# Optimization experiments

Measured on AMD Instinct MI355X. Metric: run time of the kernel, lower is better.

## Reference

```python
import jax, jax.numpy as jnp
import numpy as np

B, T, D_MODEL = 2, 2048, 2048
N, H, R = 1024, 16, 512
DH = 128          # mem_head_dim (even, fully rotated: rope_dim == DH)
MLAT = 128        # mem_latent_dim
TOPK = 64
EPS = 1e-6
ROPE_BASE = 10000.0


def _rms_norm(x, w):
    var = jnp.mean(jnp.square(x), axis=-1, keepdims=True)
    return x * jax.lax.rsqrt(var + EPS) * w


def _rotate_half(x):
    x1, x2 = jnp.split(x, 2, axis=-1)
    return jnp.concatenate([-x2, x1], axis=-1)


def _apply_rope(x, positions):
    # x: [B, H, L, DH], positions: [L] -> cos/sin [1, 1, L, DH]
    inv_freq = 1.0 / (ROPE_BASE ** (jnp.arange(0, DH, 2, dtype=jnp.float32) / DH))
    freqs = positions.astype(jnp.float32)[:, None] * inv_freq  # [L, DH/2]
    emb = jnp.concatenate([freqs, freqs], axis=-1)             # [L, DH]
    cos = jnp.cos(emb)[None, None].astype(x.dtype)
    sin = jnp.sin(emb)[None, None].astype(x.dtype)
    return x * cos + _rotate_half(x) * sin


def setup_inputs() -> dict:
    key = jax.random.key(0)
    ks = jax.random.split(key, 16)
    s = 0.02
    return {
        "x": jax.random.normal(ks[0], (B, T, D_MODEL), jnp.float32),
        "snapshots": jax.random.normal(ks[1], (B, N, H, R), jnp.float32),
        "snap_positions": jnp.sort(jax.random.randint(ks[2], (N,), 0, T)),
        "token_offset": 0,
        "Wq_down": jax.random.normal(ks[3], (D_MODEL, MLAT), jnp.float32) * s,
        "Wq_up": jax.random.normal(ks[4], (MLAT, H * DH), jnp.float32) * s,
        "Wg_down": jax.random.normal(ks[5], (D_MODEL, MLAT), jnp.float32) * s,
        "Wg_up": jax.random.normal(ks[6], (MLAT, H * DH), jnp.float32) * s,
        "Wo_down": jax.random.normal(ks[7], (H * DH, MLAT), jnp.float32) * s,
        "Wo_up": jax.random.normal(ks[8], (MLAT, D_MODEL), jnp.float32) * s,
        "Wk_up": jax.random.normal(ks[9], (R, DH), jnp.float32) * s,
        "Wv_up": jax.random.normal(ks[10], (R, DH), jnp.float32) * s,
        "q_norm_w": jnp.ones((DH,), jnp.float32),
        "k_norm_w": jnp.ones((DH,), jnp.float32),
        "sink_logit": jnp.zeros((H,), jnp.float32),
    }


def reference(x, snapshots, snap_positions, token_offset,
              Wq_down, Wq_up, Wg_down, Wg_up, Wo_down, Wo_up,
              Wk_up, Wv_up, q_norm_w, k_norm_w, sink_logit):
    b, t, d = x.shape
    _, n, h, r = snapshots.shape
    dh = DH

    # Q path: down/up projection, per-head RMSNorm -> [B, H, T, DH]
    q = ((x @ Wq_down) @ Wq_up).reshape(b, t, h, dh)
    q = _rms_norm(q, q_norm_w).transpose(0, 2, 1, 3)

    # K/V from snapshot latents: [B, N, H, DH] -> [B, H, N, DH]
    k = _rms_norm(snapshots @ Wk_up, k_norm_w).transpose(0, 2, 1, 3)
    v = (snapshots @ Wv_up).transpose(0, 2, 1, 3)

    # dual RoPE: Q by absolute token position, K by snapshot end position
    t_abs = token_offset + jnp.arange(t)
    q = _apply_rope(q, t_abs)
    k = _apply_rope(k, snap_positions)

    scores = jnp.einsum('bhtd,bhnd->bhtn', q, k) / jnp.sqrt(jnp.asarray(dh, q.dtype))

    # causal mask: snapshot strictly before token
    valid = (snap_positions[None, :] < t_abs[:, None])[None, None]  # [1,1,T,N]
    neg_inf = jnp.asarray(-jnp.inf, scores.dtype)
    scores = jnp.where(valid, scores, neg_inf)

    # causal top-k: keep entries >= k-th largest per (b,h,t)
    k_sel = min(TOPK, n)
    if k_sel < n:
        top_vals, _ = jax.lax.top_k(scores, k_sel)
        kth = top_vals[..., -1:]
        scores = jnp.where(scores >= kth, scores, neg_inf)

    # attention sink: extra learned logit per head
    sink = jnp.broadcast_to(sink_logit.astype(jnp.float32)[None, :, None, None], (b, h, t, 1))
    aug = jnp.concatenate([scores.astype(jnp.float32), sink], axis=-1)
    weights = jax.nn.softmax(aug, axis=-1)[..., :n].astype(v.dtype)

    out = jnp.einsum('bhtn,bhnd->bhtd', weights, v)
    out = out.transpose(0, 2, 1, 3).reshape(b, t, h * dh)

    gate = jax.nn.sigmoid((x @ Wg_down) @ Wg_up)
    out = out * gate
    out = (out @ Wo_down) @ Wo_up
    return out
```

## Files before the change

kernel.cpp:

```cpp
#include <hip/hip_runtime.h>

typedef unsigned short u16;
typedef unsigned int u32;
typedef __attribute__((ext_vector_type(8))) short bf16x8;
typedef __attribute__((ext_vector_type(8))) _Float16 f16x8;
typedef __attribute__((ext_vector_type(4))) float f32x4;

__device__ __forceinline__ float b2f(u16 u) {
  union { u32 i; float f; } v; v.i = ((u32)u) << 16; return v.f;
}
__device__ __forceinline__ u16 f2b(float f) {
  u32 u = __builtin_bit_cast(u32, f);
  u32 r = u + 0x7FFFu + ((u >> 16) & 1u);
  return (u16)(r >> 16);
}
__device__ __forceinline__ u16 f2h(float f) {
  return __builtin_bit_cast(u16, (_Float16)f);
}
__device__ __forceinline__ float h2f(u16 u) {
  return (float)__builtin_bit_cast(_Float16, u);
}
__device__ __forceinline__ float wsum(float v) {
  #pragma unroll
  for (int o = 32; o; o >>= 1) v += __shfl_xor(v, o);
  return v;
}

__global__ void k_detect(const u32* x, int* flag) {
  int lane = threadIdx.x;
  u32 w = x[lane * 131 + 7];
  float v = b2f((u16)(w & 0xFFFF));
  float a = fabsf(v);
  bool sane = (a > 1e-3f) && (a < 100.0f);
  unsigned long long m = __ballot(sane);
  if (lane == 0) flag[0] = (__popcll(m) >= 32) ? 0 : 1;
}

__global__ __launch_bounds__(256)
void k_tab(const int* spos, const int* tok, float2* qtab, float2* ktab, int* nmaxg) {
  if (blockIdx.x == 768) {
    int t = threadIdx.x;
    if (t < 128) {
      int lim = tok[0] + t * 16 + 15;
      int lo = 0, hi = 1024;
      #pragma unroll 1
      while (lo < hi) { int mid = (lo + hi) >> 1; if (spos[mid] < lim) lo = mid + 1; else hi = mid; }
      nmaxg[t] = lo;
    }
    return;
  }
  int id = blockIdx.x * 4 + (threadIdx.x >> 6);
  int lane = threadIdx.x & 63;
  float invf = __expf(-(float)lane * (9.210340371976184f / 64.0f));
  if (id < 2048) {
    float pos = (float)(tok[0] + id);
    float sn, cs; sincosf(pos * invf, &sn, &cs);
    qtab[id * 64 + lane] = make_float2(cs, sn);
  } else {
    int n = id - 2048;
    float pos = (float)spos[n];
    float sn, cs; sincosf(pos * invf, &sn, &cs);
    ktab[n * 64 + lane] = make_float2(cs, sn);
  }
}

struct WtArgs {
  const void* s[8];
  const void* vq; const void* vk; const void* vs;
};
__global__ __launch_bounds__(256)
void k_wtrans_all(WtArgs a, u16* wb, const int* flag) {
  __shared__ u16 Ts[64][66];
  int id = blockIdx.x, t = threadIdx.x, dt = flag[0];
  if (id == 416) {
    u16* dq = wb + 1703936; u16* dk = wb + 1704064; u16* ds = wb + 1704192;
    if (t < 128) dq[t] = dt ? f2b(((const float*)a.vq)[t]) : ((const u16*)a.vq)[t];
    else if (t < 256) dk[t-128] = dt ? f2b(((const float*)a.vk)[t-128]) : ((const u16*)a.vk)[t-128];
    if (t < 16) ds[t] = dt ? f2b(((const float*)a.vs)[t]) : ((const u16*)a.vs)[t];
    return;
  }
  const int cum[9] = {0,64,128,144,160,224,288,352,416};
  const int gsh[8] = {1,1,1,1,5,5,1,5};
  const int Ks[8]  = {2048,2048,512,512,128,128,2048,128};
  const int Ns[8]  = {128,128,128,128,2048,2048,128,2048};
  const unsigned dsts[8] = {0,262144,524288,589824,655360,917504,1179648,1441792};
  int seg = 0;
  #pragma unroll
  for (int i = 0; i < 7; ++i) seg += (id >= cum[i+1]);
  int rel = id - cum[seg];
  int bx = rel & ((1 << gsh[seg]) - 1), by = rel >> gsh[seg];
  int K = Ks[seg], N = Ns[seg];
  const void* src = a.s[seg];
  u16* dst = wb + dsts[seg];
  int col0 = bx * 64, k0 = by * 64;
  int lr = t >> 4, lc = (t & 15) * 4;
  if (dt) {
    #pragma unroll
    for (int p = 0; p < 4; ++p) {
      int kr = lr + p * 16;
      float4 v = *(const float4*)((const float*)src + (size_t)(k0 + kr) * N + col0 + lc);
      Ts[kr][lc+0] = f2b(v.x); Ts[kr][lc+1] = f2b(v.y);
      Ts[kr][lc+2] = f2b(v.z); Ts[kr][lc+3] = f2b(v.w);
    }
  } else {
    #pragma unroll
    for (int p = 0; p < 4; ++p) {
      int kr = lr + p * 16;
      uint2 v = *(const uint2*)((const u16*)src + (size_t)(k0 + kr) * N + col0 + lc);
      *(uint2*)&Ts[kr][lc] = v;
    }
  }
  __syncthreads();
  int col = t >> 2, ks = (t & 3) * 16;
  u16 tmp[16];
  #pragma unroll
  for (int i = 0; i < 16; ++i) tmp[i] = Ts[ks + i][col];
  u16* dp = dst + (size_t)(col0 + col) * K + k0 + ks;
  *(uint4*)dp = *(uint4*)&tmp[0];
  *(uint4*)(dp + 8) = *(uint4*)&tmp[8];
}

template<int JW>
__device__ __forceinline__ void skinny_body(const void* A, const u16* BT, u16* C0, u16* C1,
    int K, bool a32, int m0, int tid, u16 (*As)[40]) {
  int wave = tid >> 6, lane = tid & 63, quad = lane >> 4, l16 = lane & 15;
  f32x4 acc[JW];
  #pragma unroll
  for (int j = 0; j < JW; ++j) acc[j] = (f32x4){0.f,0.f,0.f,0.f};
  int row32 = tid >> 4, kp32 = (tid & 15) * 2;
  int row16 = tid >> 2, kp16 = (tid & 3) * 8;
  float2 pf32 = {};
  uint4 pf16 = {};
  if (a32) pf32 = *(const float2*)((const float*)A + (size_t)(m0+row32)*K + kp32);
  else if (tid < 64) pf16 = *(const uint4*)((const u16*)A + (size_t)(m0+row16)*K + kp16);
  uint4 bf[JW];
  #pragma unroll
  for (int j = 0; j < JW; ++j) {
    int col = wave*(JW*16) + j*16 + l16;
    bf[j] = *(const uint4*)(BT + (size_t)col*K + quad*8);
  }
  for (int k0 = 0; k0 < K; k0 += 32) {
    if (a32) { As[row32][kp32] = f2b(pf32.x); As[row32][kp32+1] = f2b(pf32.y); }
    else if (tid < 64) *(uint4*)&As[row16][kp16] = pf16;
    __syncthreads();
    int k1 = k0 + 32;
    uint4 bn[JW];
    if (k1 < K) {
      if (a32) pf32 = *(const float2*)((const float*)A + (size_t)(m0+row32)*K + k1 + kp32);
      else if (tid < 64) pf16 = *(const uint4*)((const u16*)A + (size_t)(m0+row16)*K + k1 + kp16);
      #pragma unroll
      for (int j = 0; j < JW; ++j) {
        int col = wave*(JW*16) + j*16 + l16;
        bn[j] = *(const uint4*)(BT + (size_t)col*K + k1 + quad*8);
      }
    }
    bf16x8 af = *(const bf16x8*)&As[l16][quad*8];
    #pragma unroll
    for (int j = 0; j < JW; ++j)
      acc[j] = __builtin_amdgcn_mfma_f32_16x16x32_bf16(af, __builtin_bit_cast(bf16x8, bf[j]), acc[j], 0, 0, 0);
    __syncthreads();
    #pragma unroll
    for (int j = 0; j < JW; ++j) bf[j] = bn[j];
  }
  #pragma unroll
  for (int j = 0; j < JW; ++j) {
    int col = wave*(JW*16) + j*16 + l16;
    u16* Cp = (col < 128) ? C0 : C1;
    int cc = col & 127;
    #pragma unroll
    for (int r = 0; r < 4; ++r)
      Cp[(size_t)(m0 + quad*4 + r)*128 + cc] = f2b(acc[j][r]);
  }
}

__device__ __forceinline__ void gemm_up_body(const u16* A, const u16* BT, void* C, int ldc,
    bool o32, int m0, int n0, int tid, u16 (*As)[40]) {
  int wave = tid >> 6, lane = tid & 63, quad = lane >> 4, l16 = lane & 15;
  f32x4 acc[4] = {};
  int row = tid >> 2, kp = (tid & 3) * 8;
  uint4 pa = *(const uint4*)(A + (size_t)(m0+row)*128 + kp);
  uint4 bf[4];
  #pragma unroll
  for (int j = 0; j < 4; ++j)
    bf[j] = *(const uint4*)(BT + (size_t)(n0 + j*16 + l16)*128 + quad*8);
  #pragma unroll
  for (int k0 = 0; k0 < 128; k0 += 32) {
    *(uint4*)&As[row][kp] = pa;
    __syncthreads();
    uint4 bn[4];
    if (k0 < 96) {
      pa = *(const uint4*)(A + (size_t)(m0+row)*128 + k0 + 32 + kp);
      #pragma unroll
      for (int j = 0; j < 4; ++j)
        bn[j] = *(const uint4*)(BT + (size_t)(n0 + j*16 + l16)*128 + k0 + 32 + quad*8);
    }
    bf16x8 af = *(const bf16x8*)&As[wave*16 + l16][quad*8];
    #pragma unroll
    for (int j = 0; j < 4; ++j)
      acc[j] = __builtin_amdgcn_mfma_f32_16x16x32_bf16(af, __builtin_bit_cast(bf16x8, bf[j]), acc[j], 0, 0, 0);
    __syncthreads();
    #pragma unroll
    for (int j = 0; j < 4; ++j) bf[j] = bn[j];
  }
  #pragma unroll
  for (int j = 0; j < 4; ++j) {
    #pragma unroll
    for (int r = 0; r < 4; ++r) {
      size_t ci = (size_t)(m0 + wave*16 + quad*4 + r)*ldc + n0 + j*16 + l16;
      float v = acc[j][r];
      if (o32) ((float*)C)[ci] = v; else ((u16*)C)[ci] = f2b(v);
    }
  }
}

__device__ __forceinline__ void kpost_body(const u16* kraw, u16* kT, const u16* kw,
                                           const float2* ktab, int rel, int tid) {
  int wave = tid >> 6, lane = tid & 63;
  int rr = rel * 4 + wave;
  int n = (rr >> 4) & 1023, b = rr >> 14, h = rr & 15;
  size_t base = (size_t)rr * 128;
  float x0 = b2f(kraw[base + lane]);
  float x1 = b2f(kraw[base + lane + 64]);
  float ss = wsum(x0*x0 + x1*x1);
  float inv = rsqrtf(ss * (1.0f/128.0f) + 1e-6f);
  float y0 = x0 * inv * b2f(kw[lane]);
  float y1 = x1 * inv * b2f(kw[lane + 64]);
  float2 cs2 = ktab[n * 64 + lane];
  size_t ob = ((size_t)(b*16 + h) * 1024 + n) * 128;
  kT[ob + lane]      = f2b(y0*cs2.x - y1*cs2.y);
  kT[ob + lane + 64] = f2b(y1*cs2.x + y0*cs2.y);
}

__device__ __forceinline__ void vtrans_body(const u16* vraw, u16* vtt, int bid, int t,
                                            u16 (*Vs)[136]) {
  int ng = bid & 15, bh = bid >> 4;
  int b = bh >> 4, h = bh & 15;
  int n0 = ng * 64;
  int li = t >> 4, seg = (t & 15) * 8;
  #pragma unroll
  for (int p = 0; p < 4; ++p) {
    int i = li + p * 16;
    size_t row = (size_t)(b*1024 + n0 + i) * 16 + h;
    *(uint4*)&Vs[i][seg] = *(const uint4*)(vraw + row*128 + seg);
  }
  __syncthreads();
  int dh = t >> 1, nh = (t & 1) * 32;
  u16 outv[32];
  #pragma unroll
  for (int i = 0; i < 32; ++i) outv[i] = f2h(b2f(Vs[nh + i][dh]));
  u16* dst = vtt + ((size_t)bh * 128 + dh) * 1024 + n0 + nh;
  *(uint4*)(dst)      = *(uint4*)&outv[0];
  *(uint4*)(dst + 8)  = *(uint4*)&outv[8];
  *(uint4*)(dst + 16) = *(uint4*)&outv[16];
  *(uint4*)(dst + 24) = *(uint4*)&outv[24];
}

__global__ __launch_bounds__(256)
void k_down_all(const void* x, const void* snap, const u16* BdT, const u16* BkvT,
                u16* qlat, u16* glat, u16* kraw, u16* vraw, const int* flag) {
  __shared__ u16 As[16][40];
  int id = blockIdx.x;
  bool a32 = flag[0] != 0;
  if (id < 256) skinny_body<4>(x, BdT, qlat, glat, 2048, a32, id*16, threadIdx.x, As);
  else          skinny_body<4>(snap, BkvT, kraw, vraw, 512, a32, (id-256)*16, threadIdx.x, As);
}

__global__ __launch_bounds__(256)
void k_mid_all(const u16* qlat, const u16* glat, const u16* WquT, const u16* WguT,
               u16* qraw, u16* graw, const u16* kraw, u16* kT, const u16* vraw, u16* vtt,
               const u16* ckw, const float2* ktab, const int* flag) {
  __shared__ u16 smem[64*136];
  int id = blockIdx.x, tid = threadIdx.x;
  if (id < 4096) {
    u16 (*As)[40] = (u16 (*)[40])smem;
    int rel = id & 2047;
    const u16* A  = (id < 2048) ? qlat : glat;
    const u16* BT = (id < 2048) ? WquT : WguT;
    u16* C        = (id < 2048) ? qraw : graw;
    gemm_up_body(A, BT, C, 2048, false, (rel >> 5) * 64, (rel & 31) * 64, tid, As);
  } else if (id < 12288) {
    kpost_body(kraw, kT, ckw, ktab, id - 4096, tid);
  } else {
    vtrans_body(vraw, vtt, id - 12288, tid, (u16 (*)[136])smem);
  }
}

__global__ __launch_bounds__(256)
void k_olat(const u16* Ao, const u16* WodT, u16* olat, const int* flag) {
  __shared__ u16 As[16][40];
  skinny_body<2>(Ao, WodT, olat, olat, 2048, false, blockIdx.x*16, threadIdx.x, As);
}

__global__ __launch_bounds__(256)
void k_gemm_up(const u16* A, const u16* BT, void* C, int ldc, const int* flag, int out_dyn) {
  __shared__ u16 As[64][40];
  gemm_up_body(A, BT, C, ldc, out_dyn && flag[0], blockIdx.y*64, blockIdx.x*64, threadIdx.x, As);
}

template<int NJ>
__device__ __forceinline__ void attn_phase2(char* scB, float* rzb, int tl0, int lane,
                                            int nmax, float sinkv, bool do_search) {
  int c0 = lane * 8;
  #pragma unroll 1
  for (int half = 0; half < 2; ++half) {
    float sv[2][NJ]; int key[2][NJ];
    #pragma unroll
    for (int s2 = 0; s2 < 2; ++s2) {
      int tl = tl0 + half*2 + s2;
      int sxor = (tl & 7) << 4;
      const char* rowp = scB + tl*2048;
      uint4 r0 = *(const uint4*)(rowp + ((lane*16) ^ sxor));
      #pragma unroll
      for (int j = 0; j < 8; ++j)
        sv[s2][j] = (c0 + j < nmax) ? h2f(((const u16*)&r0)[j]) : -INFINITY;
      if constexpr (NJ == 16) {
        uint4 r1 = *(const uint4*)(rowp + (1024 + ((lane*16) ^ sxor)));
        #pragma unroll
        for (int j = 0; j < 8; ++j)
          sv[s2][j+8] = (c0 + j + 512 < nmax) ? h2f(((const u16*)&r1)[j]) : -INFINITY;
      }
    }
    float mx[2];
    #pragma unroll
    for (int s2 = 0; s2 < 2; ++s2) {
      float m = -INFINITY;
      #pragma unroll
      for (int j = 0; j < NJ; ++j) {
        float f = sv[s2][j];
        m = fmaxf(m, f);
        float fs = fminf(fmaxf(f * 256.0f + 2048.0f, 0.0f), 4095.0f);
        key[s2][j] = (int)fs;
      }
      mx[s2] = m;
    }
    #pragma unroll
    for (int os = 32; os; os >>= 1) {
      mx[0] = fmaxf(mx[0], __shfl_xor(mx[0], os));
      mx[1] = fmaxf(mx[1], __shfl_xor(mx[1], os));
    }
    int lo2[2] = {0, 0};
    if (do_search) {
      int hi2[2] = {4096, 4096};
      #pragma unroll 1
      for (int it = 0; it < 12; ++it) {
        #pragma unroll
        for (int s2 = 0; s2 < 2; ++s2) {
          int mid = (lo2[s2] + hi2[s2]) >> 1;
          int c = 0;
          #pragma unroll
          for (int j = 0; j < NJ; ++j) c += (int)__popcll(__ballot(key[s2][j] >= mid));
          if (c >= 64) lo2[s2] = mid; else hi2[s2] = mid;
        }
      }
    }
    float m2[2], zp[2];
    u16 wq[2][16];
    #pragma unroll
    for (int s2 = 0; s2 < 2; ++s2) {
      m2[s2] = fmaxf(mx[s2], sinkv);
      float z = 0.f;
      #pragma unroll
      for (int j = 0; j < NJ; ++j) {
        float e = (key[s2][j] >= lo2[s2] && sv[s2][j] > -1e37f) ? __expf(sv[s2][j] - m2[s2]) : 0.f;
        z += e;
        wq[s2][j] = f2h(e);
      }
      zp[s2] = z;
    }
    #pragma unroll
    for (int os = 32; os; os >>= 1) {
      zp[0] += __shfl_xor(zp[0], os);
      zp[1] += __shfl_xor(zp[1], os);
    }
    #pragma unroll
    for (int s2 = 0; s2 < 2; ++s2) {
      int tl = tl0 + half*2 + s2;
      float Z = zp[s2] + __expf(sinkv - m2[s2]);
      if (lane == 0) rzb[tl] = 1.0f / Z;
      int sxor = (tl & 7) << 4;
      char* rowp = scB + tl*2048;
      *(uint4*)(rowp + ((lane*16) ^ sxor)) = *(uint4*)&wq[s2][0];
      if constexpr (NJ == 16)
        *(uint4*)(rowp + (1024 + ((lane*16) ^ sxor))) = *(uint4*)&wq[s2][8];
    }
  }
}

__global__ __launch_bounds__(256, 5)
void k_attn(const u16* qraw, const u16* kT, const u16* vtt, const u16* graw,
            const int* spos, const int* tok, const u16* sink, const u16* qw,
            const float2* qtab, const int* nmaxg, float* rzg, u16* o) {
  __shared__ u16 sc[16*1024];
  char* scB = (char*)sc;
  u16 (*Qs)[136] = (u16 (*)[136])sc;

  int tid = threadIdx.x;
  int wave = tid >> 6, lane = tid & 63, quad = lane >> 4, l16 = lane & 15;
  int bid0 = blockIdx.x;
  int bid = (bid0 & 7) * 512 + (bid0 >> 3);
  int tile = bid & 127, bh = bid >> 7;
  int h = bh & 15, b = bh >> 4;
  int t0 = tile * 16;
  int tok0 = tok[0];
  float* rzb = rzg + bid * 16;

  {
    float qw0 = b2f(qw[lane]), qw1 = b2f(qw[lane + 64]);
    #pragma unroll 1
    for (int s = 0; s < 4; ++s) {
      int i = wave*4 + s;
      size_t base = ((size_t)(b*2048 + t0 + i))*2048 + h*128;
      float x0 = b2f(qraw[base + lane]);
      float x1 = b2f(qraw[base + lane + 64]);
      float ss = wsum(x0*x0 + x1*x1);
      float inv = rsqrtf(ss * (1.0f/128.0f) + 1e-6f);
      float y0 = x0 * inv * qw0;
      float y1 = x1 * inv * qw1;
      float2 cs2 = qtab[(size_t)(t0 + i)*64 + lane];
      Qs[i][lane]      = f2b(y0*cs2.x - y1*cs2.y);
      Qs[i][lane + 64] = f2b(y1*cs2.x + y0*cs2.y);
    }
  }
  __syncthreads();

  int nmax = nmaxg[tile];
  int pmax = (nmax + 63) >> 6;
  int kkmax = (nmax + 31) >> 5;

  bf16x8 af[4];
  #pragma unroll
  for (int ks = 0; ks < 4; ++ks) af[ks] = *(const bf16x8*)&Qs[l16][ks*32 + quad*8];
  __syncthreads();

  const u16* kTb = kT + (size_t)bh * 131072;
  int nrow = wave*16 + l16;
  uint4 kf[4];
  int pn = 0;
  if (pmax > 0) {
    const u16* kr = kTb + (size_t)nrow * 128 + quad*8;
    #pragma unroll
    for (int ks = 0; ks < 4; ++ks) kf[ks] = *(const uint4*)(kr + ks*32);
    pn = spos[nrow];
  }
  int lim0 = tok0 + t0;
  #pragma unroll 1
  for (int p = 0; p < pmax; ++p) {
    uint4 kn[4];
    int pn_next = 0;
    if (p + 1 < pmax) {
      const u16* kr = kTb + (size_t)((p+1)*64 + nrow) * 128 + quad*8;
      #pragma unroll
      for (int ks = 0; ks < 4; ++ks) kn[ks] = *(const uint4*)(kr + ks*32);
      pn_next = spos[(p+1)*64 + nrow];
    }
    f32x4 c = {};
    __builtin_amdgcn_s_setprio(1);
    #pragma unroll
    for (int ks = 0; ks < 4; ++ks)
      c = __builtin_amdgcn_mfma_f32_16x16x32_bf16(af[ks], __builtin_bit_cast(bf16x8, kf[ks]), c, 0, 0, 0);
    __builtin_amdgcn_s_setprio(0);
    int n = p*64 + nrow;
    #pragma unroll
    for (int r = 0; r < 4; ++r) {
      int t = quad*4 + r;
      float s = c[r] * 0.08838834764831845f;
      if (pn >= lim0 + t) s = -INFINITY;
      *(u16*)(scB + ((t*2048 + n*2) ^ ((t&7)<<4))) = f2h(s);
    }
    #pragma unroll
    for (int ks = 0; ks < 4; ++ks) kf[ks] = kn[ks];
    pn = pn_next;
  }
  __syncthreads();

  float sinkv = b2f(sink[h]);

  int tl0 = wave*4;
  bool do_search = (nmax > 64);
  if (nmax > 512) attn_phase2<16>(scB, rzb, tl0, lane, nmax, sinkv, do_search);
  else            attn_phase2<8> (scB, rzb, tl0, lane, nmax, sinkv, do_search);
  __syncthreads();

  int dh0 = wave * 32;
  float rz4[4];
  u16 g0r[4], g1r[4];
  #pragma unroll
  for (int r = 0; r < 4; ++r) {
    int t = quad*4 + r;
    rz4[r] = rzb[t];
    size_t oi = ((size_t)(b*2048 + t0 + t))*2048 + h*128 + dh0 + l16;
    g0r[r] = graw[oi];
    g1r[r] = graw[oi + 16];
  }

  const u16* vbase = vtt + (size_t)bh * 131072;
  const u16* vr0 = vbase + (size_t)(dh0 + l16)*1024 + quad*8;
  const u16* vr1 = vbase + (size_t)(dh0 + 16 + l16)*1024 + quad*8;
  f32x4 acc0 = {}, acc1 = {};
  uint4 vf0 = *(const uint4*)vr0;
  uint4 vf1 = *(const uint4*)vr1;
  int axor = (l16&7) << 4;
  const char* arow = scB + l16*2048;
  #pragma unroll 1
  for (int kk = 0; kk < kkmax; ++kk) {
    uint4 vn0, vn1;
    if (kk + 1 < kkmax) {
      vn0 = *(const uint4*)(vr0 + (kk+1)*32);
      vn1 = *(const uint4*)(vr1 + (kk+1)*32);
    }
    f16x8 a = *(const f16x8*)(arow + ((kk*64 + quad*16) ^ axor));
    __builtin_amdgcn_s_setprio(1);
    acc0 = __builtin_amdgcn_mfma_f32_16x16x32_f16(a, __builtin_bit_cast(f16x8, vf0), acc0, 0, 0, 0);
    acc1 = __builtin_amdgcn_mfma_f32_16x16x32_f16(a, __builtin_bit_cast(f16x8, vf1), acc1, 0, 0, 0);
    __builtin_amdgcn_s_setprio(0);
    vf0 = vn0; vf1 = vn1;
  }

  #pragma unroll
  for (int r = 0; r < 4; ++r) {
    int t = quad*4 + r;
    size_t oi = ((size_t)(b*2048 + t0 + t))*2048 + h*128 + dh0 + l16;
    float g0 = 1.0f / (1.0f + __expf(-b2f(g0r[r])));
    float g1 = 1.0f / (1.0f + __expf(-b2f(g1r[r])));
    o[oi] = f2b(acc0[r] * rz4[r] * g0);
    o[oi + 16] = f2b(acc1[r] * rz4[r] * g1);
  }
}

extern "C" void kernel_launch(void* const* d_in, const int* in_sizes, int n_in,
                              void* d_out, int out_size, void* d_ws, size_t ws_size,
                              hipStream_t stream) {
  char* ws = (char*)d_ws;
  int* flag = (int*)(ws + 0);
  u16* wb = (u16*)(ws + 4096);

  u16* BdT  = wb + 0;
  u16* BkvT = wb + 524288;
  u16* WquT = wb + 655360;
  u16* WguT = wb + 917504;
  u16* WodT = wb + 1179648;
  u16* WouT = wb + 1441792;
  u16* cqw  = wb + 1703936;
  u16* ckw  = wb + 1704064;
  u16* csink= wb + 1704192;

  const size_t O_QLAT = 4198400;
  const size_t O_GLAT = 5246976;
  const size_t O_QRAW = 6295552;
  const size_t O_GRAW = 23072768;
  const size_t O_KRAW = 39849984;
  const size_t O_VRAW = 48238592;
  const size_t O_KT   = 56627200;
  const size_t O_VTT  = 65015808;
  const size_t O_QTAB = 73404416;
  const size_t O_KTAB = 74452992;
  const size_t O_NMAX = 74977280;

  const int* spos = (const int*)d_in[2];
  const int* tok  = (const int*)d_in[3];

  k_detect<<<1, 64, 0, stream>>>((const u32*)d_in[0], flag);

  k_tab<<<769, 256, 0, stream>>>(spos, tok, (float2*)(ws + O_QTAB), (float2*)(ws + O_KTAB),
      (int*)(ws + O_NMAX));

  WtArgs wa;
  wa.s[0] = d_in[4];  wa.s[1] = d_in[6];  wa.s[2] = d_in[10]; wa.s[3] = d_in[11];
  wa.s[4] = d_in[5];  wa.s[5] = d_in[7];  wa.s[6] = d_in[8];  wa.s[7] = d_in[9];
  wa.vq = d_in[12]; wa.vk = d_in[13]; wa.vs = d_in[14];
  k_wtrans_all<<<417, 256, 0, stream>>>(wa, wb, flag);

  k_down_all<<<2304, 256, 0, stream>>>(d_in[0], d_in[1], BdT, BkvT,
      (u16*)(ws + O_QLAT), (u16*)(ws + O_GLAT), (u16*)(ws + O_KRAW), (u16*)(ws + O_VRAW), flag);

  k_mid_all<<<12800, 256, 0, stream>>>((const u16*)(ws + O_QLAT), (const u16*)(ws + O_GLAT),
      WquT, WguT, (u16*)(ws + O_QRAW), (u16*)(ws + O_GRAW),
      (const u16*)(ws + O_KRAW), (u16*)(ws + O_KT), (const u16*)(ws + O_VRAW), (u16*)(ws + O_VTT),
      ckw, (const float2*)(ws + O_KTAB), flag);

  k_attn<<<4096, 256, 0, stream>>>((const u16*)(ws + O_QRAW), (const u16*)(ws + O_KT),
      (const u16*)(ws + O_VTT), (const u16*)(ws + O_GRAW), spos, tok, csink, cqw,
      (const float2*)(ws + O_QTAB), (const int*)(ws + O_NMAX),
      (float*)(ws + O_GLAT), (u16*)(ws + O_GRAW));

  k_olat<<<256, 256, 0, stream>>>((const u16*)(ws + O_GRAW), WodT, (u16*)(ws + O_QLAT), flag);
  k_gemm_up<<<dim3(32,64), 256, 0, stream>>>((const u16*)(ws + O_QLAT), WouT, d_out, 2048, flag, 1);
}
```

Before: 507.1 us.

## Halve attention tile to 8 tokens, split-K olat GEMM, fuse table kernel

The attention kernel now handles 8 query tokens per block instead of 16. It uses half the shared memory, launches twice as many blocks and raises the occupancy hint from 5 to 8. Its MFMA tiles are still 16 wide, so half the rows are duplicates and wasted. The skinny o-latent GEMM is split four ways along K into fp32 partials, followed by a small reduction kernel, to get more parallelism. The rope/nmax table kernel is merged into the weight-transpose launch to save one launch. The nmax granularity changes to 8 tokens to match the new tile size.

```diff
diff --git a/kernel.cpp b/kernel.cpp
--- a/kernel.cpp
+++ b/kernel.cpp
@@ -36,42 +36,40 @@
   if (lane == 0) flag[0] = (__popcll(m) >= 32) ? 0 : 1;
 }
 
-__global__ __launch_bounds__(256)
-void k_tab(const int* spos, const int* tok, float2* qtab, float2* ktab, int* nmaxg) {
-  if (blockIdx.x == 768) {
-    int t = threadIdx.x;
-    if (t < 128) {
-      int lim = tok[0] + t * 16 + 15;
-      int lo = 0, hi = 1024;
-      #pragma unroll 1
-      while (lo < hi) { int mid = (lo + hi) >> 1; if (spos[mid] < lim) lo = mid + 1; else hi = mid; }
-      nmaxg[t] = lo;
-    }
-    return;
-  }
-  int id = blockIdx.x * 4 + (threadIdx.x >> 6);
-  int lane = threadIdx.x & 63;
-  float invf = __expf(-(float)lane * (9.210340371976184f / 64.0f));
-  if (id < 2048) {
-    float pos = (float)(tok[0] + id);
-    float sn, cs; sincosf(pos * invf, &sn, &cs);
-    qtab[id * 64 + lane] = make_float2(cs, sn);
-  } else {
-    int n = id - 2048;
-    float pos = (float)spos[n];
-    float sn, cs; sincosf(pos * invf, &sn, &cs);
-    ktab[n * 64 + lane] = make_float2(cs, sn);
-  }
-}
-
 struct WtArgs {
   const void* s[8];
   const void* vq; const void* vk; const void* vs;
 };
 __global__ __launch_bounds__(256)
-void k_wtrans_all(WtArgs a, u16* wb, const int* flag) {
+void k_wtab(WtArgs a, u16* wb, const int* flag, const int* spos, const int* tok,
+            float2* qtab, float2* ktab, int* nmaxg) {
   __shared__ u16 Ts[64][66];
-  int id = blockIdx.x, t = threadIdx.x, dt = flag[0];
+  int id = blockIdx.x, t = threadIdx.x;
+  if (id >= 417) {
+    if (id == 1185) {
+      int lim = tok[0] + t * 8 + 7;
+      int lo = 0, hi = 1024;
+      #pragma unroll 1
+      while (lo < hi) { int mid = (lo + hi) >> 1; if (spos[mid] < lim) lo = mid + 1; else hi = mid; }
+      nmaxg[t] = lo;
+      return;
+    }
+    int rid = (id - 417) * 4 + (t >> 6);
+    int lane = t & 63;
+    float invf = __expf(-(float)lane * (9.210340371976184f / 64.0f));
+    if (rid < 2048) {
+      float pos = (float)(tok[0] + rid);
+      float sn, cs; sincosf(pos * invf, &sn, &cs);
+      qtab[rid * 64 + lane] = make_float2(cs, sn);
+    } else {
+      int n = rid - 2048;
+      float pos = (float)spos[n];
+      float sn, cs; sincosf(pos * invf, &sn, &cs);
+      ktab[n * 64 + lane] = make_float2(cs, sn);
+    }
+    return;
+  }
+  int dt = flag[0];
   if (id == 416) {
     u16* dq = wb + 1703936; u16* dk = wb + 1704064; u16* ds = wb + 1704192;
     if (t < 128) dq[t] = dt ? f2b(((const float*)a.vq)[t]) : ((const u16*)a.vq)[t];
@@ -286,9 +284,66 @@
 }
 
 __global__ __launch_bounds__(256)
-void k_olat(const u16* Ao, const u16* WodT, u16* olat, const int* flag) {
+void k_olat_part(const u16* Ao, const u16* BT, float* P) {
   __shared__ u16 As[16][40];
-  skinny_body<2>(Ao, WodT, olat, olat, 2048, false, blockIdx.x*16, threadIdx.x, As);
+  int bid = blockIdx.x;
+  int ks = bid & 3, m0 = (bid >> 2) * 16;
+  int kbase = ks * 512;
+  int tid = threadIdx.x;
+  int wave = tid >> 6, lane = tid & 63, quad = lane >> 4, l16 = lane & 15;
+  f32x4 acc[2] = {};
+  int row16 = tid >> 2, kp16 = (tid & 3) * 8;
+  uint4 pf16 = {};
+  if (tid < 64) pf16 = *(const uint4*)(Ao + (size_t)(m0+row16)*2048 + kbase + kp16);
+  uint4 bf[2];
+  #pragma unroll
+  for (int j = 0; j < 2; ++j) {
+    int col = wave*32 + j*16 + l16;
+    bf[j] = *(const uint4*)(BT + (size_t)col*2048 + kbase + quad*8);
+  }
+  for (int k0 = 0; k0 < 512; k0 += 32) {
+    if (tid < 64) *(uint4*)&As[row16][kp16] = pf16;
+    __syncthreads();
+    int k1 = k0 + 32;
+    uint4 bn[2];
+    if (k1 < 512) {
+      if (tid < 64) pf16 = *(const uint4*)(Ao + (size_t)(m0+row16)*2048 + kbase + k1 + kp16);
+      #pragma unroll
+      for (int j = 0; j < 2; ++j) {
+        int col = wave*32 + j*16 + l16;
+        bn[j] = *(const uint4*)(BT + (size_t)col*2048 + kbase + k1 + quad*8);
+      }
+    }
+    bf16x8 afr = *(const bf16x8*)&As[l16][quad*8];
+    #pragma unroll
+    for (int j = 0; j < 2; ++j)
+      acc[j] = __builtin_amdgcn_mfma_f32_16x16x32_bf16(afr, __builtin_bit_cast(bf16x8, bf[j]), acc[j], 0, 0, 0);
+    __syncthreads();
+    #pragma unroll
+    for (int j = 0; j < 2; ++j) bf[j] = bn[j];
+  }
+  #pragma unroll
+  for (int j = 0; j < 2; ++j) {
+    int col = wave*32 + j*16 + l16;
+    #pragma unroll
+    for (int r = 0; r < 4; ++r)
+      P[((size_t)ks*4096 + m0 + quad*4 + r)*128 + col] = acc[j][r];
+  }
+}
+
+__global__ __launch_bounds__(256)
+void k_osum(const float* P, u16* olat) {
+  int idx = (blockIdx.x * 256 + threadIdx.x) * 4;
+  float4 a = *(const float4*)(P + idx);
+  float4 b = *(const float4*)(P + 524288 + idx);
+  float4 c = *(const float4*)(P + 1048576 + idx);
+  float4 d = *(const float4*)(P + 1572864 + idx);
+  u16 o4[4];
+  o4[0] = f2b(((a.x + b.x) + c.x) + d.x);
+  o4[1] = f2b(((a.y + b.y) + c.y) + d.y);
+  o4[2] = f2b(((a.z + b.z) + c.z) + d.z);
+  o4[3] = f2b(((a.w + b.w) + c.w) + d.w);
+  *(uint2*)(olat + idx) = *(uint2*)&o4[0];
 }
 
 __global__ __launch_bounds__(256)
@@ -301,114 +356,114 @@
 __device__ __forceinline__ void attn_phase2(char* scB, float* rzb, int tl0, int lane,
                                             int nmax, float sinkv, bool do_search) {
   int c0 = lane * 8;
-  #pragma unroll 1
-  for (int half = 0; half < 2; ++half) {
-    float sv[2][NJ]; int key[2][NJ];
-    #pragma unroll
-    for (int s2 = 0; s2 < 2; ++s2) {
-      int tl = tl0 + half*2 + s2;
-      int sxor = (tl & 7) << 4;
-      const char* rowp = scB + tl*2048;
-      uint4 r0 = *(const uint4*)(rowp + ((lane*16) ^ sxor));
+  float sv[2][NJ]; int key[2][NJ];
+  #pragma unroll
+  for (int s2 = 0; s2 < 2; ++s2) {
+    int tl = tl0 + s2;
+    int sxor = (tl & 7) << 4;
+    const char* rowp = scB + tl*2048;
+    uint4 r0 = *(const uint4*)(rowp + ((lane*16) ^ sxor));
+    if constexpr (NJ == 16) {
+      #pragma unroll
+      for (int j = 0; j < 8; ++j) sv[s2][j] = h2f(((const u16*)&r0)[j]);
+      uint4 r1 = *(const uint4*)(rowp + (1024 + ((lane*16) ^ sxor)));
+      #pragma unroll
+      for (int j = 0; j < 8; ++j)
+        sv[s2][j+8] = (c0 + j + 512 < nmax) ? h2f(((const u16*)&r1)[j]) : -INFINITY;
+    } else {
       #pragma unroll
       for (int j = 0; j < 8; ++j)
         sv[s2][j] = (c0 + j < nmax) ? h2f(((const u16*)&r0)[j]) : -INFINITY;
-      if constexpr (NJ == 16) {
-        uint4 r1 = *(const uint4*)(rowp + (1024 + ((lane*16) ^ sxor)));
+    }
+  }
+  float mx[2];
+  #pragma unroll
+  for (int s2 = 0; s2 < 2; ++s2) {
+    float m = -INFINITY;
+    #pragma unroll
+    for (int j = 0; j < NJ; ++j) {
+      float f = sv[s2][j];
+      m = fmaxf(m, f);
+      float fs = fminf(fmaxf(f * 256.0f + 2048.0f, 0.0f), 4095.0f);
+      key[s2][j] = (int)fs;
+    }
+    mx[s2] = m;
+  }
+  #pragma unroll
+  for (int os = 32; os; os >>= 1) {
+    mx[0] = fmaxf(mx[0], __shfl_xor(mx[0], os));
+    mx[1] = fmaxf(mx[1], __shfl_xor(mx[1], os));
+  }
+  int lo2[2] = {0, 0};
+  if (do_search) {
+    int hi2[2] = {4096, 4096};
+    #pragma unroll 1
+    for (int it = 0; it < 12; ++it) {
+      #pragma unroll
+      for (int s2 = 0; s2 < 2; ++s2) {
+        int mid = (lo2[s2] + hi2[s2]) >> 1;
+        int c = 0;
         #pragma unroll
-        for (int j = 0; j < 8; ++j)
-          sv[s2][j+8] = (c0 + j + 512 < nmax) ? h2f(((const u16*)&r1)[j]) : -INFINITY;
+        for (int j = 0; j < NJ; ++j) c += (int)__popcll(__ballot(key[s2][j] >= mid));
+        if (c >= 64) lo2[s2] = mid; else hi2[s2] = mid;
       }
     }
-    float mx[2];
-    #pragma unroll
-    for (int s2 = 0; s2 < 2; ++s2) {
-      float m = -INFINITY;
-      #pragma unroll
-      for (int j = 0; j < NJ; ++j) {
-        float f = sv[s2][j];
-        m = fmaxf(m, f);
-        float fs = fminf(fmaxf(f * 256.0f + 2048.0f, 0.0f), 4095.0f);
-        key[s2][j] = (int)fs;
-      }
-      mx[s2] = m;
-    }
-    #pragma unroll
-    for (int os = 32; os; os >>= 1) {
-      mx[0] = fmaxf(mx[0], __shfl_xor(mx[0], os));
-      mx[1] = fmaxf(mx[1], __shfl_xor(mx[1], os));
-    }
-    int lo2[2] = {0, 0};
-    if (do_search) {
-      int hi2[2] = {4096, 4096};
-      #pragma unroll 1
-      for (int it = 0; it < 12; ++it) {
-        #pragma unroll
-        for (int s2 = 0; s2 < 2; ++s2) {
-          int mid = (lo2[s2] + hi2[s2]) >> 1;
-          int c = 0;
-          #pragma unroll
-          for (int j = 0; j < NJ; ++j) c += (int)__popcll(__ballot(key[s2][j] >= mid));
-          if (c >= 64) lo2[s2] = mid; else hi2[s2] = mid;
-        }
-      }
-    }
-    float m2[2], zp[2];
-    u16 wq[2][16];
-    #pragma unroll
-    for (int s2 = 0; s2 < 2; ++s2) {
-      m2[s2] = fmaxf(mx[s2], sinkv);
-      float z = 0.f;
-      #pragma unroll
-      for (int j = 0; j < NJ; ++j) {
-        float e = (key[s2][j] >= lo2[s2] && sv[s2][j] > -1e37f) ? __expf(sv[s2][j] - m2[s2]) : 0.f;
-        z += e;
-        wq[s2][j] = f2h(e);
-      }
-      zp[s2] = z;
-    }
-    #pragma unroll
-    for (int os = 32; os; os >>= 1) {
-      zp[0] += __shfl_xor(zp[0], os);
-      zp[1] += __shfl_xor(zp[1], os);
-    }
-    #pragma unroll
-    for (int s2 = 0; s2 < 2; ++s2) {
-      int tl = tl0 + half*2 + s2;
-      float Z = zp[s2] + __expf(sinkv - m2[s2]);
-      if (lane == 0) rzb[tl] = 1.0f / Z;
-      int sxor = (tl & 7) << 4;
-      char* rowp = scB + tl*2048;
-      *(uint4*)(rowp + ((lane*16) ^ sxor)) = *(uint4*)&wq[s2][0];
-      if constexpr (NJ == 16)
-        *(uint4*)(rowp + (1024 + ((lane*16) ^ sxor))) = *(uint4*)&wq[s2][8];
-    }
-  }
-}
-
-__global__ __launch_bounds__(256, 5)
+  }
+  float m2[2], zp[2];
+  u16 wq[2][16];
+  #pragma unroll
+  for (int s2 = 0; s2 < 2; ++s2) {
+    m2[s2] = fmaxf(mx[s2], sinkv);
+    float z = 0.f;
+    #pragma unroll
+    for (int j = 0; j < NJ; ++j) {
+      float e = (key[s2][j] >= lo2[s2] && sv[s2][j] > -1e37f) ? __expf(sv[s2][j] - m2[s2]) : 0.f;
+      z += e;
+      wq[s2][j] = f2h(e);
+    }
+    zp[s2] = z;
+  }
+  #pragma unroll
+  for (int os = 32; os; os >>= 1) {
+    zp[0] += __shfl_xor(zp[0], os);
+    zp[1] += __shfl_xor(zp[1], os);
+  }
+  #pragma unroll
+  for (int s2 = 0; s2 < 2; ++s2) {
+    int tl = tl0 + s2;
+    float Z = zp[s2] + __expf(sinkv - m2[s2]);
+    if (lane == 0) rzb[tl] = 1.0f / Z;
+    int sxor = (tl & 7) << 4;
+    char* rowp = scB + tl*2048;
+    *(uint4*)(rowp + ((lane*16) ^ sxor)) = *(uint4*)&wq[s2][0];
+    if constexpr (NJ == 16)
+      *(uint4*)(rowp + (1024 + ((lane*16) ^ sxor))) = *(uint4*)&wq[s2][8];
+  }
+}
+
+__global__ __launch_bounds__(256, 8)
 void k_attn(const u16* qraw, const u16* kT, const u16* vtt, const u16* graw,
             const int* spos, const int* tok, const u16* sink, const u16* qw,
             const float2* qtab, const int* nmaxg, float* rzg, u16* o) {
-  __shared__ u16 sc[16*1024];
+  __shared__ u16 sc[8*1024];
   char* scB = (char*)sc;
   u16 (*Qs)[136] = (u16 (*)[136])sc;
 
   int tid = threadIdx.x;
   int wave = tid >> 6, lane = tid & 63, quad = lane >> 4, l16 = lane & 15;
   int bid0 = blockIdx.x;
-  int bid = (bid0 & 7) * 512 + (bid0 >> 3);
-  int tile = bid & 127, bh = bid >> 7;
+  int bid = (bid0 & 7) * 1024 + (bid0 >> 3);
+  int tile = bid & 255, bh = bid >> 8;
   int h = bh & 15, b = bh >> 4;
-  int t0 = tile * 16;
+  int t0 = tile * 8;
   int tok0 = tok[0];
   float* rzb = rzg + bid * 16;
 
   {
     float qw0 = b2f(qw[lane]), qw1 = b2f(qw[lane + 64]);
     #pragma unroll 1
-    for (int s = 0; s < 4; ++s) {
-      int i = wave*4 + s;
+    for (int s = 0; s < 2; ++s) {
+      int i = wave*2 + s;
       size_t base = ((size_t)(b*2048 + t0 + i))*2048 + h*128;
       float x0 = b2f(qraw[base + lane]);
       float x1 = b2f(qraw[base + lane + 64]);
@@ -429,7 +484,7 @@
 
   bf16x8 af[4];
   #pragma unroll
-  for (int ks = 0; ks < 4; ++ks) af[ks] = *(const bf16x8*)&Qs[l16][ks*32 + quad*8];
+  for (int ks = 0; ks < 4; ++ks) af[ks] = *(const bf16x8*)&Qs[l16 & 7][ks*32 + quad*8];
   __syncthreads();
 
   const u16* kTb = kT + (size_t)bh * 131072;
@@ -460,12 +515,14 @@
       c = __builtin_amdgcn_mfma_f32_16x16x32_bf16(af[ks], __builtin_bit_cast(bf16x8, kf[ks]), c, 0, 0, 0);
     __builtin_amdgcn_s_setprio(0);
     int n = p*64 + nrow;
-    #pragma unroll
-    for (int r = 0; r < 4; ++r) {
-      int t = quad*4 + r;
-      float s = c[r] * 0.08838834764831845f;
-      if (pn >= lim0 + t) s = -INFINITY;
-      *(u16*)(scB + ((t*2048 + n*2) ^ ((t&7)<<4))) = f2h(s);
+    if (quad < 2) {
+      #pragma unroll
+      for (int r = 0; r < 4; ++r) {
+        int t = quad*4 + r;
+        float s = c[r] * 0.08838834764831845f;
+        if (pn >= lim0 + t) s = -INFINITY;
+        *(u16*)(scB + ((t*2048 + n*2) ^ ((t&7)<<4))) = f2h(s);
+      }
     }
     #pragma unroll
     for (int ks = 0; ks < 4; ++ks) kf[ks] = kn[ks];
@@ -475,7 +532,7 @@
 
   float sinkv = b2f(sink[h]);
 
-  int tl0 = wave*4;
+  int tl0 = wave*2;
   bool do_search = (nmax > 64);
   if (nmax > 512) attn_phase2<16>(scB, rzb, tl0, lane, nmax, sinkv, do_search);
   else            attn_phase2<8> (scB, rzb, tl0, lane, nmax, sinkv, do_search);
@@ -484,13 +541,15 @@
   int dh0 = wave * 32;
   float rz4[4];
   u16 g0r[4], g1r[4];
-  #pragma unroll
-  for (int r = 0; r < 4; ++r) {
-    int t = quad*4 + r;
-    rz4[r] = rzb[t];
-    size_t oi = ((size_t)(b*2048 + t0 + t))*2048 + h*128 + dh0 + l16;
-    g0r[r] = graw[oi];
-    g1r[r] = graw[oi + 16];
+  if (quad < 2) {
+    #pragma unroll
+    for (int r = 0; r < 4; ++r) {
+      int t = quad*4 + r;
+      rz4[r] = rzb[t];
+      size_t oi = ((size_t)(b*2048 + t0 + t))*2048 + h*128 + dh0 + l16;
+      g0r[r] = graw[oi];
+      g1r[r] = graw[oi + 16];
+    }
   }
 
   const u16* vbase = vtt + (size_t)bh * 131072;
@@ -499,8 +558,8 @@
   f32x4 acc0 = {}, acc1 = {};
   uint4 vf0 = *(const uint4*)vr0;
   uint4 vf1 = *(const uint4*)vr1;
-  int axor = (l16&7) << 4;
-  const char* arow = scB + l16*2048;
+  int axor = (l16 & 7) << 4;
+  const char* arow = scB + (l16 & 7)*2048;
   #pragma unroll 1
   for (int kk = 0; kk < kkmax; ++kk) {
     uint4 vn0, vn1;
@@ -516,14 +575,16 @@
     vf0 = vn0; vf1 = vn1;
   }
 
-  #pragma unroll
-  for (int r = 0; r < 4; ++r) {
-    int t = quad*4 + r;
-    size_t oi = ((size_t)(b*2048 + t0 + t))*2048 + h*128 + dh0 + l16;
-    float g0 = 1.0f / (1.0f + __expf(-b2f(g0r[r])));
-    float g1 = 1.0f / (1.0f + __expf(-b2f(g1r[r])));
-    o[oi] = f2b(acc0[r] * rz4[r] * g0);
-    o[oi + 16] = f2b(acc1[r] * rz4[r] * g1);
+  if (quad < 2) {
+    #pragma unroll
+    for (int r = 0; r < 4; ++r) {
+      int t = quad*4 + r;
+      size_t oi = ((size_t)(b*2048 + t0 + t))*2048 + h*128 + dh0 + l16;
+      float g0 = 1.0f / (1.0f + __expf(-b2f(g0r[r])));
+      float g1 = 1.0f / (1.0f + __expf(-b2f(g1r[r])));
+      o[oi] = f2b(acc0[r] * rz4[r] * g0);
+      o[oi + 16] = f2b(acc1[r] * rz4[r] * g1);
+    }
   }
 }
 
@@ -561,14 +622,12 @@
 
   k_detect<<<1, 64, 0, stream>>>((const u32*)d_in[0], flag);
 
-  k_tab<<<769, 256, 0, stream>>>(spos, tok, (float2*)(ws + O_QTAB), (float2*)(ws + O_KTAB),
-      (int*)(ws + O_NMAX));
-
   WtArgs wa;
   wa.s[0] = d_in[4];  wa.s[1] = d_in[6];  wa.s[2] = d_in[10]; wa.s[3] = d_in[11];
   wa.s[4] = d_in[5];  wa.s[5] = d_in[7];  wa.s[6] = d_in[8];  wa.s[7] = d_in[9];
   wa.vq = d_in[12]; wa.vk = d_in[13]; wa.vs = d_in[14];
-  k_wtrans_all<<<417, 256, 0, stream>>>(wa, wb, flag);
+  k_wtab<<<1186, 256, 0, stream>>>(wa, wb, flag, spos, tok,
+      (float2*)(ws + O_QTAB), (float2*)(ws + O_KTAB), (int*)(ws + O_NMAX));
 
   k_down_all<<<2304, 256, 0, stream>>>(d_in[0], d_in[1], BdT, BkvT,
       (u16*)(ws + O_QLAT), (u16*)(ws + O_GLAT), (u16*)(ws + O_KRAW), (u16*)(ws + O_VRAW), flag);
@@ -578,11 +637,12 @@
       (const u16*)(ws + O_KRAW), (u16*)(ws + O_KT), (const u16*)(ws + O_VRAW), (u16*)(ws + O_VTT),
       ckw, (const float2*)(ws + O_KTAB), flag);
 
-  k_attn<<<4096, 256, 0, stream>>>((const u16*)(ws + O_QRAW), (const u16*)(ws + O_KT),
+  k_attn<<<8192, 256, 0, stream>>>((const u16*)(ws + O_QRAW), (const u16*)(ws + O_KT),
       (const u16*)(ws + O_VTT), (const u16*)(ws + O_GRAW), spos, tok, csink, cqw,
       (const float2*)(ws + O_QTAB), (const int*)(ws + O_NMAX),
       (float*)(ws + O_GLAT), (u16*)(ws + O_GRAW));
 
-  k_olat<<<256, 256, 0, stream>>>((const u16*)(ws + O_GRAW), WodT, (u16*)(ws + O_QLAT), flag);
+  k_olat_part<<<1024, 256, 0, stream>>>((const u16*)(ws + O_GRAW), WodT, (float*)(ws + O_KRAW));
+  k_osum<<<512, 256, 0, stream>>>((const float*)(ws + O_KRAW), (u16*)(ws + O_QLAT));
   k_gemm_up<<<dim3(32,64), 256, 0, stream>>>((const u16*)(ws + O_QLAT), WouT, d_out, 2048, flag, 1);
 }
```

Measured after the change: 633.1 us. 24.8% more time.
